# Optimization experiments

Hardware: AMD Instinct MI355X
Metric: run time of the kernel (lower is better)

Reference implementation:

```python
import jax, jax.numpy as jnp
import numpy as np

RATIO = 0.1

def setup_inputs() -> dict:
    key = jax.random.key(0)
    x = jax.random.normal(key, (8, 1024, 4096), dtype=jnp.float32)
    return {"x": x}

def reference(x):
    shape = x.shape
    xf = x.reshape(-1)                       # [N]
    k = int(RATIO * xf.shape[0])             # static k
    src, index = jax.lax.top_k(xf, k)         # values (not abs), matching torch.topk
    out = jnp.zeros_like(xf).at[index].set(src)
    return out.reshape(shape)
```

## Files before the change

### kernel.cpp

```cpp
#include <hip/hip_runtime.h>
#include <hip/hip_bf16.h>
#include <stdint.h>


#define STREAM_GRID 1024
#define STREAM_BLK  256
#define EQ_CAP      65536


__device__ __forceinline__ unsigned int f2u(float x) {
    unsigned int b = __float_as_uint(x);
    return (b & 0x80000000u) ? ~b : (b | 0x80000000u);
}

__global__ void init_kernel(unsigned int* sc, unsigned int k) {
    if (threadIdx.x == 0) {
        sc[0] = 0u; sc[1] = k; sc[2] = 0u; sc[3] = 0u; sc[4] = 0u;
    }
}

__global__ void __launch_bounds__(256)
hist_lds_kernel(const float* __restrict__ x, int n4, long long N,
                unsigned int* __restrict__ hist,
                const unsigned int* __restrict__ sc,
                int nbins, int shift, int match_shift)
{
    __shared__ unsigned int lh[4][2048];
    int tid = threadIdx.x;
    for (int i = tid; i < 4 * 2048; i += 256) ((unsigned int*)lh)[i] = 0u;
    const bool filt = (match_shift < 32);
    const int ms = filt ? match_shift : 0;
    unsigned int pref = 0u;
    if (filt) pref = sc[0] >> ms;
    __syncthreads();
    unsigned int* my = lh[tid >> 6];
    const float4* x4 = (const float4*)x;
    const unsigned int mask = (unsigned int)nbins - 1u;
    int stride = gridDim.x * blockDim.x;
    for (int i = blockIdx.x * blockDim.x + tid; i < n4; i += stride) {
        float4 v = x4[i];
        unsigned int u;
        u = f2u(v.x); if (!filt || ((u >> ms) == pref)) atomicAdd(&my[(u >> shift) & mask], 1u);
        u = f2u(v.y); if (!filt || ((u >> ms) == pref)) atomicAdd(&my[(u >> shift) & mask], 1u);
        u = f2u(v.z); if (!filt || ((u >> ms) == pref)) atomicAdd(&my[(u >> shift) & mask], 1u);
        u = f2u(v.w); if (!filt || ((u >> ms) == pref)) atomicAdd(&my[(u >> shift) & mask], 1u);
    }
    long long t0 = (long long)n4 * 4;
    if (blockIdx.x == 0 && tid < (int)(N - t0)) {
        unsigned int u = f2u(x[t0 + tid]);
        if (!filt || ((u >> ms) == pref)) atomicAdd(&my[(u >> shift) & mask], 1u);
    }
    __syncthreads();
    for (int i = tid; i < nbins; i += 256) {
        unsigned int s = lh[0][i] + lh[1][i] + lh[2][i] + lh[3][i];
        if (s) atomicAdd(&hist[i], s);
    }
}

__global__ void __launch_bounds__(256)
hist21_kernel(const float* __restrict__ x, int n4, long long N,
              unsigned int* __restrict__ hist2,
              const unsigned int* __restrict__ sc)
{
    unsigned int b1 = sc[0] >> 21;
    const float4* x4 = (const float4*)x;
    int stride = gridDim.x * blockDim.x;
    for (int i = blockIdx.x * blockDim.x + threadIdx.x; i < n4; i += stride) {
        float4 v = x4[i];
        unsigned int u;
        u = f2u(v.x); if ((u >> 21) == b1) atomicAdd(&hist2[u & 0x1FFFFFu], 1u);
        u = f2u(v.y); if ((u >> 21) == b1) atomicAdd(&hist2[u & 0x1FFFFFu], 1u);
        u = f2u(v.z); if ((u >> 21) == b1) atomicAdd(&hist2[u & 0x1FFFFFu], 1u);
        u = f2u(v.w); if ((u >> 21) == b1) atomicAdd(&hist2[u & 0x1FFFFFu], 1u);
    }
    long long t0 = (long long)n4 * 4;
    if (blockIdx.x == 0 && threadIdx.x < (int)(N - t0)) {
        unsigned int u = f2u(x[t0 + threadIdx.x]);
        if ((u >> 21) == b1) atomicAdd(&hist2[u & 0x1FFFFFu], 1u);
    }
}

__device__ __forceinline__ unsigned int block_exscan256(unsigned int v,
                                                        volatile unsigned int* lds,
                                                        int tid)
{
    lds[tid] = v;
    __syncthreads();
    for (int off = 1; off < 256; off <<= 1) {
        unsigned int t = (tid >= off) ? lds[tid - off] : 0u;
        __syncthreads();
        lds[tid] += t;
        __syncthreads();
    }
    unsigned int incl = lds[tid];
    return incl - v;
}

__global__ void __launch_bounds__(256)
scan_kernel(unsigned int* __restrict__ hist, int nbins, int shift, int is_final,
            unsigned int* __restrict__ sc)
{
    __shared__ unsigned int lds[256];
    int tid = threadIdx.x;
    int seg = nbins >> 8;
    unsigned int prefix = sc[0];
    unsigned int krem = sc[1];
    unsigned int loc[8];
    unsigned int partial = 0u;
    for (int i = 0; i < seg; ++i) {
        int p = tid * seg + i;
        unsigned int v = hist[nbins - 1 - p];
        loc[i] = v; partial += v;
    }
    unsigned int cum = block_exscan256(partial, lds, tid);
    for (int i = 0; i < seg; ++i) {
        int p = tid * seg + i;
        int bin = nbins - 1 - p;
        unsigned int c = loc[i];
        if (cum < krem && cum + c >= krem) {
            if (is_final) { sc[2] = prefix | ((unsigned int)bin << shift); sc[3] = krem - cum; }
            else          { sc[0] = prefix | ((unsigned int)bin << shift); sc[1] = krem - cum; }
        }
        cum += c;
    }
    for (int i = 0; i < seg; ++i) hist[nbins - 1 - (tid * seg + i)] = 0u;
}

__global__ void __launch_bounds__(256)
chunksum_kernel(const unsigned int* __restrict__ hist2, unsigned int* __restrict__ chunk_sums)
{
    __shared__ unsigned int p[256];
    int tid = threadIdx.x;
    int chunk = blockIdx.x;
    const unsigned int* base = hist2 + (size_t)chunk * 1024;
    unsigned int s = 0u;
    for (int i = tid; i < 1024; i += 256) s += base[i];
    p[tid] = s;
    __syncthreads();
    for (int off = 128; off; off >>= 1) {
        if (tid < off) p[tid] += p[tid + off];
        __syncthreads();
    }
    if (tid == 0) chunk_sums[chunk] = p[0];
}

__global__ void __launch_bounds__(256)
scanA_final_kernel(const unsigned int* __restrict__ hist2,
                   const unsigned int* __restrict__ chunk_sums,
                   unsigned int* __restrict__ sc)
{
    __shared__ unsigned int lds[256];
    __shared__ unsigned int s_c, s_krem2;
    int tid = threadIdx.x;
    unsigned int prefix = sc[0];
    unsigned int krem = sc[1];
    unsigned int loc[8];
    unsigned int partial = 0u;
    for (int i = 0; i < 8; ++i) {
        int p = tid * 8 + i;
        unsigned int v = chunk_sums[2047 - p];
        loc[i] = v; partial += v;
    }
    unsigned int cum = block_exscan256(partial, lds, tid);
    for (int i = 0; i < 8; ++i) {
        int p = tid * 8 + i;
        int chunk = 2047 - p;
        unsigned int c = loc[i];
        if (cum < krem && cum + c >= krem) { s_c = (unsigned int)chunk; s_krem2 = krem - cum; }
        cum += c;
    }
    __syncthreads();
    unsigned int c = s_c;
    unsigned int krem2 = s_krem2;
    unsigned int loc2[4];
    partial = 0u;
    for (int i = 0; i < 4; ++i) {
        int p = tid * 4 + i;
        unsigned int v = hist2[(size_t)c * 1024 + (1023 - p)];
        loc2[i] = v; partial += v;
    }
    __syncthreads();
    unsigned int cum2 = block_exscan256(partial, lds, tid);
    for (int i = 0; i < 4; ++i) {
        int p = tid * 4 + i;
        int bin = 1023 - p;
        unsigned int cc = loc2[i];
        if (cum2 < krem2 && cum2 + cc >= krem2) {
            sc[2] = prefix | (c * 1024u + (unsigned int)bin);
            sc[3] = krem2 - cum2;
        }
        cum2 += cc;
    }
}

__global__ void __launch_bounds__(256)
scatter_kernel(const float* __restrict__ x, int n4, long long N,
               float* __restrict__ out,
               unsigned int* __restrict__ sc,
               unsigned int* __restrict__ eq_list, int cap)
{
    unsigned int tu = sc[2];
    const float4* x4 = (const float4*)x;
    float4* o4 = (float4*)out;
    int stride = gridDim.x * blockDim.x;
    for (int i = blockIdx.x * blockDim.x + threadIdx.x; i < n4; i += stride) {
        float4 v = x4[i];
        unsigned int u0 = f2u(v.x), u1 = f2u(v.y), u2 = f2u(v.z), u3 = f2u(v.w);
        float4 o;
        o.x = (u0 > tu) ? v.x : 0.0f;
        o.y = (u1 > tu) ? v.y : 0.0f;
        o.z = (u2 > tu) ? v.z : 0.0f;
        o.w = (u3 > tu) ? v.w : 0.0f;
        if (u0 == tu || u1 == tu || u2 == tu || u3 == tu) {
            unsigned int b = (unsigned int)i * 4u;
            if (u0 == tu) { unsigned int p = atomicAdd(&sc[4], 1u); if (p < (unsigned int)cap) eq_list[p] = b + 0u; }
            if (u1 == tu) { unsigned int p = atomicAdd(&sc[4], 1u); if (p < (unsigned int)cap) eq_list[p] = b + 1u; }
            if (u2 == tu) { unsigned int p = atomicAdd(&sc[4], 1u); if (p < (unsigned int)cap) eq_list[p] = b + 2u; }
            if (u3 == tu) { unsigned int p = atomicAdd(&sc[4], 1u); if (p < (unsigned int)cap) eq_list[p] = b + 3u; }
        }
        o4[i] = o;
    }
    long long t0 = (long long)n4 * 4;
    if (blockIdx.x == 0 && threadIdx.x < (int)(N - t0)) {
        long long idx = t0 + threadIdx.x;
        float v = x[idx];
        unsigned int u = f2u(v);
        out[idx] = (u > tu) ? v : 0.0f;
        if (u == tu) { unsigned int p = atomicAdd(&sc[4], 1u); if (p < (unsigned int)cap) eq_list[p] = (unsigned int)idx; }
    }
}

__global__ void __launch_bounds__(256)
eqfix_kernel(float* __restrict__ out, const unsigned int* __restrict__ sc,
             const unsigned int* __restrict__ eq_list, int cap)
{
    unsigned int m = sc[4];
    if (m > (unsigned int)cap) m = (unsigned int)cap;
    unsigned int need = sc[3];
    unsigned int tu = sc[2];
    float f = __uint_as_float((tu & 0x80000000u) ? (tu & 0x7FFFFFFFu) : ~tu);
    for (unsigned int j = threadIdx.x; j < m; j += blockDim.x) {
        unsigned int idx = eq_list[j];
        unsigned int cnt = 0u;
        for (unsigned int l = 0; l < m; ++l) cnt += (eq_list[l] < idx) ? 1u : 0u;
        if (cnt < need) out[idx] = f;
    }
}

extern "C" void kernel_launch(void* const* d_in, const int* in_sizes, int n_in,
                              void* d_out, int out_size, void* d_ws, size_t ws_size,
                              hipStream_t stream) {
    const float* x = (const float*)d_in[0];
    float* out = (float*)d_out;
    long long N = (long long)in_sizes[0];
    int n4 = (int)(N >> 2);
    unsigned int k = (unsigned int)((double)N * 0.1);
    if (k == 0u) k = 1u;

    uint8_t* w = (uint8_t*)d_ws;
    unsigned int* sc         = (unsigned int*)(w);
    unsigned int* hist1      = (unsigned int*)(w + 256);
    unsigned int* chunk_sums = (unsigned int*)(w + 256 + 8192);
    unsigned int* eq_list    = (unsigned int*)(w + 256 + 16384);
    size_t baseB = 256 + 16384 + 262144;
    unsigned int* hist2      = (unsigned int*)(w + baseB);
    size_t needA = baseB + ((size_t)1 << 21) * sizeof(unsigned int);
    bool planA = (ws_size >= needA);

    int grid = STREAM_GRID;

    hipMemsetAsync(hist1, 0, 2048 * sizeof(unsigned int), stream);
    init_kernel<<<1, 64, 0, stream>>>(sc, k);

    if (planA) {
        hipMemsetAsync(hist2, 0, ((size_t)1 << 21) * sizeof(unsigned int), stream);
        hist_lds_kernel<<<grid, STREAM_BLK, 0, stream>>>(x, n4, N, hist1, sc, 2048, 21, 32);
        scan_kernel<<<1, 256, 0, stream>>>(hist1, 2048, 21, 0, sc);
        hist21_kernel<<<grid, STREAM_BLK, 0, stream>>>(x, n4, N, hist2, sc);
        chunksum_kernel<<<2048, 256, 0, stream>>>(hist2, chunk_sums);
        scanA_final_kernel<<<1, 256, 0, stream>>>(hist2, chunk_sums, sc);
    } else {
        hist_lds_kernel<<<grid, STREAM_BLK, 0, stream>>>(x, n4, N, hist1, sc, 2048, 21, 32);
        scan_kernel<<<1, 256, 0, stream>>>(hist1, 2048, 21, 0, sc);
        hist_lds_kernel<<<grid, STREAM_BLK, 0, stream>>>(x, n4, N, hist1, sc, 2048, 10, 21);
        scan_kernel<<<1, 256, 0, stream>>>(hist1, 2048, 10, 0, sc);
        hist_lds_kernel<<<grid, STREAM_BLK, 0, stream>>>(x, n4, N, hist1, sc, 1024, 0, 10);
        scan_kernel<<<1, 256, 0, stream>>>(hist1, 1024, 0, 1, sc);
    }

    scatter_kernel<<<grid, STREAM_BLK, 0, stream>>>(x, n4, N, out, sc, eq_list, EQ_CAP);
    eqfix_kernel<<<1, 256, 0, stream>>>(out, sc, eq_list, EQ_CAP);
}
```

Baseline: 331.6 us.

## Estimate threshold by sampling, then single-pass windowed fine histogram with fallback

After: 1.082 ms. 226% more time.

```diff
diff --git a/kernel.cpp b/kernel.cpp
--- a/kernel.cpp
+++ b/kernel.cpp
@@ -1,209 +1,257 @@
 #include <hip/hip_runtime.h>
-#include <hip/hip_bf16.h>
 #include <stdint.h>
 
 
-#define STREAM_GRID 1024
-#define STREAM_BLK  256
-#define EQ_CAP      65536
-
+#define EQ_CAP 65536
+
+#define SC_WLO   0
+#define SC_K     1
+#define SC_TU    2
+#define SC_NEED  3
+#define SC_EQN   4
+#define SC_OK    5
+#define SC_ABOVE 6
+#define SC_DONE1 7
+#define SC_DONE2 8
+#define SC_FBHI  9
+#define SC_FBKR  10
 
 __device__ __forceinline__ unsigned int f2u(float x) {
     unsigned int b = __float_as_uint(x);
     return (b & 0x80000000u) ? ~b : (b | 0x80000000u);
 }
-
-__global__ void init_kernel(unsigned int* sc, unsigned int k) {
-    if (threadIdx.x == 0) {
-        sc[0] = 0u; sc[1] = k; sc[2] = 0u; sc[3] = 0u; sc[4] = 0u;
-    }
-}
-
-__global__ void __launch_bounds__(256)
-hist_lds_kernel(const float* __restrict__ x, int n4, long long N,
-                unsigned int* __restrict__ hist,
-                const unsigned int* __restrict__ sc,
-                int nbins, int shift, int match_shift)
-{
-    __shared__ unsigned int lh[4][2048];
-    int tid = threadIdx.x;
-    for (int i = tid; i < 4 * 2048; i += 256) ((unsigned int*)lh)[i] = 0u;
-    const bool filt = (match_shift < 32);
-    const int ms = filt ? match_shift : 0;
-    unsigned int pref = 0u;
-    if (filt) pref = sc[0] >> ms;
-    __syncthreads();
-    unsigned int* my = lh[tid >> 6];
+__device__ __forceinline__ float u2f(unsigned int u) {
+    return __uint_as_float((u & 0x80000000u) ? (u & 0x7FFFFFFFu) : ~u);
+}
+
+__device__ __forceinline__ unsigned int block_exscan256(unsigned int v,
+                                                        unsigned int* lds,
+                                                        int tid)
+{
+    lds[tid] = v;
+    __syncthreads();
+    for (int off = 1; off < 256; off <<= 1) {
+        unsigned int t = (tid >= off) ? lds[tid - off] : 0u;
+        __syncthreads();
+        lds[tid] += t;
+        __syncthreads();
+    }
+    return lds[tid] - v;
+}
+
+__global__ void __launch_bounds__(1024)
+sample_kernel(const float* __restrict__ x, long long N, unsigned int k,
+              unsigned int* __restrict__ sc, unsigned int wbits)
+{
+    __shared__ unsigned int lh[2048];
+    __shared__ unsigned int s_u;
+    int tid = threadIdx.x;
+    for (int i = tid; i < 2048; i += 1024) lh[i] = 0u;
+    __syncthreads();
+    const int NS = 65536;
+    long long stride = N / NS; if (stride < 1) stride = 1;
+    for (int it = 0; it < NS / 1024; ++it) {
+        long long idx = (long long)(tid + it * 1024) * stride;
+        if (idx < N) {
+            unsigned int u = f2u(x[idx]);
+            atomicAdd(&lh[u >> 21], 1u);
+        }
+    }
+    __syncthreads();
+    if (tid < 64) {
+        unsigned int part = 0u;
+        for (int j = 0; j < 32; ++j) part += lh[2047 - (tid * 32 + j)];
+        unsigned int incl = part;
+        for (int o = 1; o < 64; o <<= 1) {
+            unsigned int t = __shfl_up(incl, o, 64);
+            if (tid >= o) incl += t;
+        }
+        unsigned int ex = incl - part;
+        unsigned int ks = (unsigned int)((double)NS * (double)k / (double)N);
+        if (ks < 1u) ks = 1u;
+        unsigned int cum = ex;
+        for (int j = 0; j < 32; ++j) {
+            int bin = 2047 - (tid * 32 + j);
+            unsigned int c = lh[bin];
+            if (cum < ks && cum + c >= ks)
+                s_u = ((unsigned int)bin << 21) | (1u << 20);
+            cum += c;
+        }
+    }
+    __syncthreads();
+    if (tid == 0) {
+        unsigned int wsize = 1u << wbits;
+        unsigned int half = wsize >> 1;
+        unsigned int uhat = s_u;
+        unsigned int wlo = (uhat > half) ? (uhat - half) : 0u;
+        unsigned int wlomax = (unsigned int)(0u - wsize);
+        if (wlo > wlomax) wlo = wlomax;
+        sc[SC_WLO] = wlo;  sc[SC_K] = k;
+        sc[SC_TU] = 0u;    sc[SC_NEED] = 0u;  sc[SC_EQN] = 0u;
+        sc[SC_OK] = 0u;    sc[SC_ABOVE] = 0u;
+        sc[SC_DONE1] = 0u; sc[SC_DONE2] = 0u;
+        sc[SC_FBHI] = 0u;  sc[SC_FBKR] = 0u;
+    }
+}
+
+__global__ void __launch_bounds__(256)
+main_kernel(const float* __restrict__ x, int n4, long long N,
+            unsigned int* __restrict__ fine,
+            unsigned int* __restrict__ fbz,
+            unsigned int* __restrict__ sc, unsigned int wbits)
+{
+    int tid = threadIdx.x;
+    int g = blockIdx.x * blockDim.x + tid;
+    if (g < 131072) fbz[g] = 0u;
+    unsigned int wlo = sc[SC_WLO];
+    unsigned int whiM1 = wlo + (1u << wbits) - 1u;
     const float4* x4 = (const float4*)x;
-    const unsigned int mask = (unsigned int)nbins - 1u;
     int stride = gridDim.x * blockDim.x;
-    for (int i = blockIdx.x * blockDim.x + tid; i < n4; i += stride) {
+    unsigned int above = 0u;
+    for (int i = g; i < n4; i += stride) {
         float4 v = x4[i];
         unsigned int u;
-        u = f2u(v.x); if (!filt || ((u >> ms) == pref)) atomicAdd(&my[(u >> shift) & mask], 1u);
-        u = f2u(v.y); if (!filt || ((u >> ms) == pref)) atomicAdd(&my[(u >> shift) & mask], 1u);
-        u = f2u(v.z); if (!filt || ((u >> ms) == pref)) atomicAdd(&my[(u >> shift) & mask], 1u);
-        u = f2u(v.w); if (!filt || ((u >> ms) == pref)) atomicAdd(&my[(u >> shift) & mask], 1u);
+        u = f2u(v.x); if (u > whiM1) ++above; else if (u >= wlo) atomicAdd(&fine[u - wlo], 1u);
+        u = f2u(v.y); if (u > whiM1) ++above; else if (u >= wlo) atomicAdd(&fine[u - wlo], 1u);
+        u = f2u(v.z); if (u > whiM1) ++above; else if (u >= wlo) atomicAdd(&fine[u - wlo], 1u);
+        u = f2u(v.w); if (u > whiM1) ++above; else if (u >= wlo) atomicAdd(&fine[u - wlo], 1u);
     }
     long long t0 = (long long)n4 * 4;
     if (blockIdx.x == 0 && tid < (int)(N - t0)) {
         unsigned int u = f2u(x[t0 + tid]);
-        if (!filt || ((u >> ms) == pref)) atomicAdd(&my[(u >> shift) & mask], 1u);
-    }
-    __syncthreads();
-    for (int i = tid; i < nbins; i += 256) {
-        unsigned int s = lh[0][i] + lh[1][i] + lh[2][i] + lh[3][i];
-        if (s) atomicAdd(&hist[i], s);
-    }
-}
-
-__global__ void __launch_bounds__(256)
-hist21_kernel(const float* __restrict__ x, int n4, long long N,
-              unsigned int* __restrict__ hist2,
-              const unsigned int* __restrict__ sc)
-{
-    unsigned int b1 = sc[0] >> 21;
+        if (u > whiM1) ++above; else if (u >= wlo) atomicAdd(&fine[u - wlo], 1u);
+    }
+    for (int o = 32; o; o >>= 1) above += __shfl_down(above, o, 64);
+    if ((tid & 63) == 0 && above) atomicAdd(&sc[SC_ABOVE], above);
+}
+
+__global__ void __launch_bounds__(256)
+scan_fine_kernel(const unsigned int* __restrict__ fine,
+                 unsigned int* __restrict__ chunk_sums,
+                 unsigned int* __restrict__ sc)
+{
+    __shared__ unsigned int lds[256];
+    __shared__ unsigned int sh[4];
+    __shared__ unsigned int s_total;
+    int tid = threadIdx.x;
+    int nchunk = gridDim.x;
+    const unsigned int* base = fine + (size_t)blockIdx.x * 1024;
+    unsigned int s = 0u;
+    for (int i = tid; i < 1024; i += 256) s += base[i];
+    lds[tid] = s;
+    __syncthreads();
+    for (int o = 128; o; o >>= 1) { if (tid < o) lds[tid] += lds[tid + o]; __syncthreads(); }
+    if (tid == 0) chunk_sums[blockIdx.x] = lds[0];
+    __threadfence();
+    if (tid == 0) {
+        unsigned int old = atomicAdd(&sc[SC_DONE1], 1u);
+        sh[0] = (old == (unsigned int)(nchunk - 1)) ? 1u : 0u;
+    }
+    __syncthreads();
+    if (!sh[0]) return;
+    __threadfence();
+    unsigned int k = sc[SC_K];
+    unsigned int above = sc[SC_ABOVE];
+    int seg = nchunk >> 8;
+    unsigned int part = 0u;
+    for (int j = 0; j < seg; ++j) part += chunk_sums[nchunk - 1 - (tid * seg + j)];
+    unsigned int ex = block_exscan256(part, lds, tid);
+    if (tid == 255) s_total = ex + part;
+    __syncthreads();
+    unsigned int total = s_total;
+    unsigned int valid = (above < k) && ((k - above) <= total);
+    if (tid == 0) sc[SC_OK] = valid;
+    if (!valid) return;
+    unsigned int krem = k - above;
+    unsigned int cum = ex;
+    for (int j = 0; j < seg; ++j) {
+        int c = nchunk - 1 - (tid * seg + j);
+        unsigned int cc = chunk_sums[c];
+        if (cum < krem && cum + cc >= krem) { sh[1] = (unsigned int)c; sh[2] = krem - cum; }
+        cum += cc;
+    }
+    __syncthreads();
+    unsigned int C = sh[1], krem2 = sh[2];
+    unsigned int loc[4]; unsigned int p2 = 0u;
+    for (int j = 0; j < 4; ++j) {
+        unsigned int v = fine[(size_t)C * 1024 + (1023 - (tid * 4 + j))];
+        loc[j] = v; p2 += v;
+    }
+    __syncthreads();
+    unsigned int ex2 = block_exscan256(p2, lds, tid);
+    unsigned int cum2 = ex2;
+    for (int j = 0; j < 4; ++j) {
+        int bin = 1023 - (tid * 4 + j);
+        unsigned int cc = loc[j];
+        if (cum2 < krem2 && cum2 + cc >= krem2) {
+            sc[SC_TU] = sc[SC_WLO] + C * 1024u + (unsigned int)bin;
+            sc[SC_NEED] = krem2 - cum2;
+        }
+        cum2 += cc;
+    }
+}
+
+__global__ void __launch_bounds__(256)
+fb_hist_kernel(const float* __restrict__ x, int n4, long long N,
+               unsigned int* __restrict__ hist,
+               const unsigned int* __restrict__ sc, int lowpass)
+{
+    if (sc[SC_OK]) return;
+    unsigned int pref = lowpass ? sc[SC_FBHI] : 0u;
     const float4* x4 = (const float4*)x;
     int stride = gridDim.x * blockDim.x;
     for (int i = blockIdx.x * blockDim.x + threadIdx.x; i < n4; i += stride) {
         float4 v = x4[i];
         unsigned int u;
-        u = f2u(v.x); if ((u >> 21) == b1) atomicAdd(&hist2[u & 0x1FFFFFu], 1u);
-        u = f2u(v.y); if ((u >> 21) == b1) atomicAdd(&hist2[u & 0x1FFFFFu], 1u);
-        u = f2u(v.z); if ((u >> 21) == b1) atomicAdd(&hist2[u & 0x1FFFFFu], 1u);
-        u = f2u(v.w); if ((u >> 21) == b1) atomicAdd(&hist2[u & 0x1FFFFFu], 1u);
+        #define FB_ONE(c) u = f2u(c); \
+            if (!lowpass) atomicAdd(&hist[u >> 16], 1u); \
+            else if ((u >> 16) == pref) atomicAdd(&hist[u & 0xFFFFu], 1u);
+        FB_ONE(v.x) FB_ONE(v.y) FB_ONE(v.z) FB_ONE(v.w)
+        #undef FB_ONE
     }
     long long t0 = (long long)n4 * 4;
     if (blockIdx.x == 0 && threadIdx.x < (int)(N - t0)) {
         unsigned int u = f2u(x[t0 + threadIdx.x]);
-        if ((u >> 21) == b1) atomicAdd(&hist2[u & 0x1FFFFFu], 1u);
-    }
-}
-
-__device__ __forceinline__ unsigned int block_exscan256(unsigned int v,
-                                                        volatile unsigned int* lds,
-                                                        int tid)
-{
-    lds[tid] = v;
-    __syncthreads();
-    for (int off = 1; off < 256; off <<= 1) {
-        unsigned int t = (tid >= off) ? lds[tid - off] : 0u;
-        __syncthreads();
-        lds[tid] += t;
-        __syncthreads();
-    }
-    unsigned int incl = lds[tid];
-    return incl - v;
-}
-
-__global__ void __launch_bounds__(256)
-scan_kernel(unsigned int* __restrict__ hist, int nbins, int shift, int is_final,
-            unsigned int* __restrict__ sc)
-{
+        if (!lowpass) atomicAdd(&hist[u >> 16], 1u);
+        else if ((u >> 16) == pref) atomicAdd(&hist[u & 0xFFFFu], 1u);
+    }
+}
+
+__global__ void __launch_bounds__(256)
+fb_scan_kernel(const unsigned int* __restrict__ hist,
+               unsigned int* __restrict__ sc, int lowpass)
+{
+    if (sc[SC_OK]) return;
     __shared__ unsigned int lds[256];
     int tid = threadIdx.x;
-    int seg = nbins >> 8;
-    unsigned int prefix = sc[0];
-    unsigned int krem = sc[1];
-    unsigned int loc[8];
-    unsigned int partial = 0u;
-    for (int i = 0; i < seg; ++i) {
-        int p = tid * seg + i;
-        unsigned int v = hist[nbins - 1 - p];
-        loc[i] = v; partial += v;
-    }
-    unsigned int cum = block_exscan256(partial, lds, tid);
-    for (int i = 0; i < seg; ++i) {
-        int p = tid * seg + i;
-        int bin = nbins - 1 - p;
-        unsigned int c = loc[i];
-        if (cum < krem && cum + c >= krem) {
-            if (is_final) { sc[2] = prefix | ((unsigned int)bin << shift); sc[3] = krem - cum; }
-            else          { sc[0] = prefix | ((unsigned int)bin << shift); sc[1] = krem - cum; }
-        }
-        cum += c;
-    }
-    for (int i = 0; i < seg; ++i) hist[nbins - 1 - (tid * seg + i)] = 0u;
-}
-
-__global__ void __launch_bounds__(256)
-chunksum_kernel(const unsigned int* __restrict__ hist2, unsigned int* __restrict__ chunk_sums)
-{
-    __shared__ unsigned int p[256];
-    int tid = threadIdx.x;
-    int chunk = blockIdx.x;
-    const unsigned int* base = hist2 + (size_t)chunk * 1024;
-    unsigned int s = 0u;
-    for (int i = tid; i < 1024; i += 256) s += base[i];
-    p[tid] = s;
-    __syncthreads();
-    for (int off = 128; off; off >>= 1) {
-        if (tid < off) p[tid] += p[tid + off];
-        __syncthreads();
-    }
-    if (tid == 0) chunk_sums[chunk] = p[0];
-}
-
-__global__ void __launch_bounds__(256)
-scanA_final_kernel(const unsigned int* __restrict__ hist2,
-                   const unsigned int* __restrict__ chunk_sums,
-                   unsigned int* __restrict__ sc)
-{
-    __shared__ unsigned int lds[256];
-    __shared__ unsigned int s_c, s_krem2;
-    int tid = threadIdx.x;
-    unsigned int prefix = sc[0];
-    unsigned int krem = sc[1];
-    unsigned int loc[8];
-    unsigned int partial = 0u;
-    for (int i = 0; i < 8; ++i) {
-        int p = tid * 8 + i;
-        unsigned int v = chunk_sums[2047 - p];
-        loc[i] = v; partial += v;
-    }
-    unsigned int cum = block_exscan256(partial, lds, tid);
-    for (int i = 0; i < 8; ++i) {
-        int p = tid * 8 + i;
-        int chunk = 2047 - p;
-        unsigned int c = loc[i];
-        if (cum < krem && cum + c >= krem) { s_c = (unsigned int)chunk; s_krem2 = krem - cum; }
-        cum += c;
-    }
-    __syncthreads();
-    unsigned int c = s_c;
-    unsigned int krem2 = s_krem2;
-    unsigned int loc2[4];
-    partial = 0u;
-    for (int i = 0; i < 4; ++i) {
-        int p = tid * 4 + i;
-        unsigned int v = hist2[(size_t)c * 1024 + (1023 - p)];
-        loc2[i] = v; partial += v;
-    }
-    __syncthreads();
-    unsigned int cum2 = block_exscan256(partial, lds, tid);
-    for (int i = 0; i < 4; ++i) {
-        int p = tid * 4 + i;
-        int bin = 1023 - p;
-        unsigned int cc = loc2[i];
-        if (cum2 < krem2 && cum2 + cc >= krem2) {
-            sc[2] = prefix | (c * 1024u + (unsigned int)bin);
-            sc[3] = krem2 - cum2;
-        }
-        cum2 += cc;
+    unsigned int krem = lowpass ? sc[SC_FBKR] : sc[SC_K];
+    unsigned int part = 0u;
+    for (int j = 0; j < 256; ++j) part += hist[65535 - (tid * 256 + j)];
+    unsigned int ex = block_exscan256(part, lds, tid);
+    unsigned int cum = ex;
+    for (int j = 0; j < 256; ++j) {
+        int bin = 65535 - (tid * 256 + j);
+        unsigned int cc = hist[bin];
+        if (cum < krem && cum + cc >= krem) {
+            if (!lowpass) { sc[SC_FBHI] = (unsigned int)bin; sc[SC_FBKR] = krem - cum; }
+            else { sc[SC_TU] = (sc[SC_FBHI] << 16) | (unsigned int)bin; sc[SC_NEED] = krem - cum; }
+        }
+        cum += cc;
     }
 }
 
 __global__ void __launch_bounds__(256)
 scatter_kernel(const float* __restrict__ x, int n4, long long N,
-               float* __restrict__ out,
-               unsigned int* __restrict__ sc,
+               float* __restrict__ out, unsigned int* __restrict__ sc,
                unsigned int* __restrict__ eq_list, int cap)
 {
-    unsigned int tu = sc[2];
+    __shared__ unsigned int s_last;
+    int tid = threadIdx.x;
+    unsigned int tu = sc[SC_TU];
     const float4* x4 = (const float4*)x;
     float4* o4 = (float4*)out;
     int stride = gridDim.x * blockDim.x;
-    for (int i = blockIdx.x * blockDim.x + threadIdx.x; i < n4; i += stride) {
+    for (int i = blockIdx.x * blockDim.x + tid; i < n4; i += stride) {
         float4 v = x4[i];
         unsigned int u0 = f2u(v.x), u1 = f2u(v.y), u2 = f2u(v.z), u3 = f2u(v.w);
         float4 o;
@@ -213,33 +261,34 @@
         o.w = (u3 > tu) ? v.w : 0.0f;
         if (u0 == tu || u1 == tu || u2 == tu || u3 == tu) {
             unsigned int b = (unsigned int)i * 4u;
-            if (u0 == tu) { unsigned int p = atomicAdd(&sc[4], 1u); if (p < (unsigned int)cap) eq_list[p] = b + 0u; }
-            if (u1 == tu) { unsigned int p = atomicAdd(&sc[4], 1u); if (p < (unsigned int)cap) eq_list[p] = b + 1u; }
-            if (u2 == tu) { unsigned int p = atomicAdd(&sc[4], 1u); if (p < (unsigned int)cap) eq_list[p] = b + 2u; }
-            if (u3 == tu) { unsigned int p = atomicAdd(&sc[4], 1u); if (p < (unsigned int)cap) eq_list[p] = b + 3u; }
+            if (u0 == tu) { unsigned int p = atomicAdd(&sc[SC_EQN], 1u); if (p < (unsigned int)cap) eq_list[p] = b + 0u; }
+            if (u1 == tu) { unsigned int p = atomicAdd(&sc[SC_EQN], 1u); if (p < (unsigned int)cap) eq_list[p] = b + 1u; }
+            if (u2 == tu) { unsigned int p = atomicAdd(&sc[SC_EQN], 1u); if (p < (unsigned int)cap) eq_list[p] = b + 2u; }
+            if (u3 == tu) { unsigned int p = atomicAdd(&sc[SC_EQN], 1u); if (p < (unsigned int)cap) eq_list[p] = b + 3u; }
         }
         o4[i] = o;
     }
     long long t0 = (long long)n4 * 4;
-    if (blockIdx.x == 0 && threadIdx.x < (int)(N - t0)) {
-        long long idx = t0 + threadIdx.x;
+    if (blockIdx.x == 0 && tid < (int)(N - t0)) {
+        long long idx = t0 + tid;
         float v = x[idx];
         unsigned int u = f2u(v);
         out[idx] = (u > tu) ? v : 0.0f;
-        if (u == tu) { unsigned int p = atomicAdd(&sc[4], 1u); if (p < (unsigned int)cap) eq_list[p] = (unsigned int)idx; }
-    }
-}
-
-__global__ void __launch_bounds__(256)
-eqfix_kernel(float* __restrict__ out, const unsigned int* __restrict__ sc,
-             const unsigned int* __restrict__ eq_list, int cap)
-{
-    unsigned int m = sc[4];
-    if (m > (unsigned int)cap) m = (unsigned int)cap;
-    unsigned int need = sc[3];
-    unsigned int tu = sc[2];
-    float f = __uint_as_float((tu & 0x80000000u) ? (tu & 0x7FFFFFFFu) : ~tu);
-    for (unsigned int j = threadIdx.x; j < m; j += blockDim.x) {
+        if (u == tu) { unsigned int p = atomicAdd(&sc[SC_EQN], 1u); if (p < (unsigned int)cap) eq_list[p] = (unsigned int)idx; }
+    }
+    __threadfence();
+    __syncthreads();
+    if (tid == 0) {
+        unsigned int old = atomicAdd(&sc[SC_DONE2], 1u);
+        s_last = (old == gridDim.x - 1u) ? 1u : 0u;
+    }
+    __syncthreads();
+    if (!s_last) return;
+    __threadfence();
+    unsigned int m = sc[SC_EQN]; if (m > (unsigned int)cap) m = (unsigned int)cap;
+    unsigned int need = sc[SC_NEED];
+    float f = u2f(tu);
+    for (unsigned int j = tid; j < m; j += 256) {
         unsigned int idx = eq_list[j];
         unsigned int cnt = 0u;
         for (unsigned int l = 0; l < m; ++l) cnt += (eq_list[l] < idx) ? 1u : 0u;
@@ -257,37 +306,27 @@
     unsigned int k = (unsigned int)((double)N * 0.1);
     if (k == 0u) k = 1u;
 
+    unsigned int wbits = 22;
+    if (ws_size < (1u << 20) + ((size_t)4u << 22)) wbits = 19;
+
     uint8_t* w = (uint8_t*)d_ws;
-    unsigned int* sc         = (unsigned int*)(w);
-    unsigned int* hist1      = (unsigned int*)(w + 256);
-    unsigned int* chunk_sums = (unsigned int*)(w + 256 + 8192);
-    unsigned int* eq_list    = (unsigned int*)(w + 256 + 16384);
-    size_t baseB = 256 + 16384 + 262144;
-    unsigned int* hist2      = (unsigned int*)(w + baseB);
-    size_t needA = baseB + ((size_t)1 << 21) * sizeof(unsigned int);
-    bool planA = (ws_size >= needA);
-
-    int grid = STREAM_GRID;
-
-    hipMemsetAsync(hist1, 0, 2048 * sizeof(unsigned int), stream);
-    init_kernel<<<1, 64, 0, stream>>>(sc, k);
-
-    if (planA) {
-        hipMemsetAsync(hist2, 0, ((size_t)1 << 21) * sizeof(unsigned int), stream);
-        hist_lds_kernel<<<grid, STREAM_BLK, 0, stream>>>(x, n4, N, hist1, sc, 2048, 21, 32);
-        scan_kernel<<<1, 256, 0, stream>>>(hist1, 2048, 21, 0, sc);
-        hist21_kernel<<<grid, STREAM_BLK, 0, stream>>>(x, n4, N, hist2, sc);
-        chunksum_kernel<<<2048, 256, 0, stream>>>(hist2, chunk_sums);
-        scanA_final_kernel<<<1, 256, 0, stream>>>(hist2, chunk_sums, sc);
-    } else {
-        hist_lds_kernel<<<grid, STREAM_BLK, 0, stream>>>(x, n4, N, hist1, sc, 2048, 21, 32);
-        scan_kernel<<<1, 256, 0, stream>>>(hist1, 2048, 21, 0, sc);
-        hist_lds_kernel<<<grid, STREAM_BLK, 0, stream>>>(x, n4, N, hist1, sc, 2048, 10, 21);
-        scan_kernel<<<1, 256, 0, stream>>>(hist1, 2048, 10, 0, sc);
-        hist_lds_kernel<<<grid, STREAM_BLK, 0, stream>>>(x, n4, N, hist1, sc, 1024, 0, 10);
-        scan_kernel<<<1, 256, 0, stream>>>(hist1, 1024, 0, 1, sc);
-    }
-
-    scatter_kernel<<<grid, STREAM_BLK, 0, stream>>>(x, n4, N, out, sc, eq_list, EQ_CAP);
-    eqfix_kernel<<<1, 256, 0, stream>>>(out, sc, eq_list, EQ_CAP);
-}
+    unsigned int* sc         = (unsigned int*)w;
+    unsigned int* chunk_sums = (unsigned int*)(w + 1024);
+    unsigned int* fbz        = (unsigned int*)(w + 32768);
+    unsigned int* fbA        = fbz;
+    unsigned int* fbB        = fbz + 65536;
+    unsigned int* eq_list    = (unsigned int*)(w + 32768 + 524288);
+    unsigned int* fine       = (unsigned int*)(w + (1u << 20));
+
+    int nchunk = 1 << (wbits - 10);
+
+    hipMemsetAsync(fine, 0, ((size_t)4u << wbits), stream);
+    sample_kernel<<<1, 1024, 0, stream>>>(x, N, k, sc, wbits);
+    main_kernel<<<2048, 256, 0, stream>>>(x, n4, N, fine, fbz, sc, wbits);
+    scan_fine_kernel<<<nchunk, 256, 0, stream>>>(fine, chunk_sums, sc);
+    fb_hist_kernel<<<1024, 256, 0, stream>>>(x, n4, N, fbA, sc, 0);
+    fb_scan_kernel<<<1, 256, 0, stream>>>(fbA, sc, 0);
+    fb_hist_kernel<<<1024, 256, 0, stream>>>(x, n4, N, fbB, sc, 1);
+    fb_scan_kernel<<<1, 256, 0, stream>>>(fbB, sc, 1);
+    scatter_kernel<<<2048, 256, 0, stream>>>(x, n4, N, out, sc, eq_list, EQ_CAP);
+}
```
